# Optimization experiments

Measured on AMD Instinct MI355X. Metric: run time of the kernel, lower is better.

## Reference

```python
import jax, jax.numpy as jnp
import numpy as np

B, NB, K, S = 4, 131072, 32, 768


def setup_inputs() -> dict:
    key = jax.random.key(0)
    k1, k2, k3, k4 = jax.random.split(key, 4)
    N = B * NB
    logits_embedding = jax.random.normal(k1, (N, 4), dtype=jnp.float32)
    logits_seediness = jax.random.normal(k2, (N, 1), dtype=jnp.float32)
    coords = jax.random.uniform(k3, (N, 3), dtype=jnp.float32, minval=0.0, maxval=float(S))
    inst = jax.random.randint(k4, (N,), 0, K).astype(jnp.float32)
    batch = jnp.repeat(jnp.arange(B, dtype=jnp.float32), NB)
    labels = jnp.concatenate(
        [batch[:, None], coords, jnp.zeros((N, 1), jnp.float32), inst[:, None]], axis=1)
    return {"logits_embedding": logits_embedding,
            "logits_seediness": logits_seediness,
            "labels": labels}


def reference(logits_embedding, logits_seediness, labels):
    half = S / 2.0
    # coords_embedding = emb[:, :3] + (voxel_coords - S/2) / (S/2)
    ce = logits_embedding[:, :3] + (labels[:, 1:4] - half) / half          # [N,3]
    sigma = logits_embedding[:, 3]                                          # [N]
    seed = logits_seediness.reshape(-1)                                     # [N]
    inst = labels[:, 5].astype(jnp.int32)                                   # [N]

    # batch ids are contiguous by construction -> reshape to [B, NB, ...]
    ce = ce.reshape(B, NB, 3)
    sigma = sigma.reshape(B, NB)
    seed = seed.reshape(B, NB)
    inst = inst.reshape(B, NB)

    onehot = (inst[:, :, None] == jnp.arange(K)[None, None, :]).astype(jnp.float32)  # [B,NB,K]
    counts = jnp.maximum(onehot.sum(axis=1), 1.0)                                    # [B,K]

    centers = jnp.einsum('bnk,bnd->bkd', onehot, ce) / counts[:, :, None]            # [B,K,3]
    sigmas = jnp.einsum('bnk,bn->bk', onehot, sigma) / counts                        # [B,K]

    # squared distance of every point to every instance center
    diff = ce[:, :, None, :] - centers[:, None, :, :]                                # [B,NB,K,3]
    dist2 = jnp.sum(diff * diff, axis=-1)                                            # [B,NB,K]

    arg = jnp.clip(dist2 / (2.0 * sigmas[:, None, :] ** 2), 1e-7, 100.0)
    p = jnp.exp(-arg)                                                                # [B,NB,K]

    # mask loss: log(p) == -arg exactly
    mask_loss = -(onehot * (-arg) + (1.0 - onehot) * jnp.log1p(-p)).sum(axis=(1, 2)) / NB / K  # [B]

    smooth = (onehot * jnp.abs(sigma[:, :, None] - sigmas[:, None, :])).sum(axis=1) / counts
    smooth_loss = smooth.sum(axis=1) / K                                             # [B]

    seed_term = (onehot * (seed[:, :, None] - p) ** 2).sum(axis=1) / counts
    seed_loss = seed_term.sum(axis=1) / K                                            # [B]

    # inter-cluster hinge, sum over unordered pairs i<j, denom K*(K-1)
    cdiff = centers[:, :, None, :] - centers[:, None, :, :]                          # [B,K,K,3]
    cd2 = jnp.sum(cdiff * cdiff, axis=-1)
    eye = jnp.eye(K, dtype=jnp.float32)[None]
    d = jnp.sqrt(jnp.where(eye > 0, 1.0, cd2))                                       # safe sqrt on diag
    hinge = jnp.maximum(0.0, 2.0 * 0.5 - d) ** 2 * (1.0 - eye)
    inter_loss = hinge.sum(axis=(1, 2)) / 2.0 / (K * (K - 1))                        # [B]

    loss = jnp.mean(mask_loss + smooth_loss + inter_loss + seed_loss)

    # accuracy: assign each point to nearest center (instance ids are 0..K-1)
    pred = jnp.argmin(dist2, axis=2)                                                 # [B,NB]
    acc = jnp.mean((pred == inst).astype(jnp.float32))
    return loss, jax.lax.stop_gradient(acc)
```

## Files before the change

### kernel.cpp

```cpp
#include <hip/hip_runtime.h>

#define B_ 4
#define NB_ 131072
#define K_ 32
#define N_ (B_*NB_)
#define BK_ (B_*K_)
#define NACC 256
#define ABLK 64
#define PTS_PER_ACC 2048

#define ACC_OFF  0
#define FIN_OFF  (NACC*5*K_)
#define PART_OFF (FIN_OFF + 6*BK_)

__global__ __launch_bounds__(1024) void k_accum(
    const float4* __restrict__ emb, const float* __restrict__ labels,
    float* __restrict__ ws)
{
    __shared__ float sacc[5*K_];
    int tid = threadIdx.x;
    if (tid < 5*K_) sacc[tid] = 0.f;
    __syncthreads();
    int start = blockIdx.x * PTS_PER_ACC;
    #pragma unroll
    for (int i = 0; i < PTS_PER_ACC/1024; ++i) {
        int n = start + i*1024 + tid;
        float4 e = emb[n];
        const float* lr = labels + (size_t)n*6;
        float c1 = lr[1];
        float2 c23 = *reinterpret_cast<const float2*>(lr + 2);
        int inst = ((int)lr[5]) & 31;
        float cex = e.x + (c1    - 384.f)/384.f;
        float cey = e.y + (c23.x - 384.f)/384.f;
        float cez = e.z + (c23.y - 384.f)/384.f;
        atomicAdd(&sacc[0*K_+inst], cex);
        atomicAdd(&sacc[1*K_+inst], cey);
        atomicAdd(&sacc[2*K_+inst], cez);
        atomicAdd(&sacc[3*K_+inst], e.w);
        atomicAdd(&sacc[4*K_+inst], 1.0f);
    }
    __syncthreads();
    if (tid < 5*K_) ws[ACC_OFF + blockIdx.x*5*K_ + tid] = sacc[tid];
}

__global__ __launch_bounds__(256) void k_main(
    const float4* __restrict__ emb, const float* __restrict__ seedp,
    const float* __restrict__ labels, float* __restrict__ ws,
    float4* __restrict__ part)
{
    __shared__ float s_raw[5*K_];
    __shared__ float s_cx[K_], s_cy[K_], s_cz[K_], s_sig[K_], s_inv[K_], s_i2s[K_];
    int tid = threadIdx.x;
    int n = blockIdx.x * 256 + tid;
    int b = blockIdx.x >> 9;

    if (tid < 5*K_) {
        float a = 0.f;
        const float* base = ws + ACC_OFF + (size_t)b*ABLK*5*K_ + tid;
        #pragma unroll 8
        for (int j = 0; j < ABLK; ++j) a += base[(size_t)j*5*K_];
        s_raw[tid] = a;
    }
    __syncthreads();
    if (tid < K_) {
        float cnt = fmaxf(s_raw[4*K_+tid], 1.f);
        float inv = 1.f / cnt;
        float cx = s_raw[0*K_+tid] * inv;
        float cy = s_raw[1*K_+tid] * inv;
        float cz = s_raw[2*K_+tid] * inv;
        float sg = s_raw[3*K_+tid] * inv;
        float i2s = 1.f / (2.f*sg*sg);
        s_cx[tid] = cx;  s_cy[tid] = cy;  s_cz[tid] = cz;
        s_sig[tid] = sg; s_inv[tid] = inv; s_i2s[tid] = i2s;
        if ((blockIdx.x & 511) == 0) {
            float* fin = ws + FIN_OFF;
            fin[0*BK_ + b*K_+tid] = cx;
            fin[1*BK_ + b*K_+tid] = cy;
            fin[2*BK_ + b*K_+tid] = cz;
            fin[3*BK_ + b*K_+tid] = sg;
            fin[4*BK_ + b*K_+tid] = inv;
            fin[5*BK_ + b*K_+tid] = i2s;
        }
    }
    __syncthreads();

    float4 e = emb[n];
    float sd = seedp[n];
    const float* lr = labels + (size_t)n*6;
    float c1 = lr[1];
    float2 c23 = *reinterpret_cast<const float2*>(lr + 2);
    int inst = ((int)lr[5]) & 31;
    float cex = e.x + (c1    - 384.f)/384.f;
    float cey = e.y + (c23.x - 384.f)/384.f;
    float cez = e.z + (c23.y - 384.f)/384.f;
    float sigma = e.w;

    unsigned bestpk = 0xffffffffu;
    float minarg = 3.4e38f;
    #pragma unroll
    for (int k = 0; k < K_; ++k) {
        float dx = cex - s_cx[k];
        float dy = cey - s_cy[k];
        float dz = cez - s_cz[k];
        float d2 = dx*dx + dy*dy + dz*dz;
        unsigned pk = (__float_as_uint(d2) & ~31u) | (unsigned)k;
        bestpk = min(bestpk, pk);
        minarg = fminf(minarg, d2 * s_i2s[k]);
    }
    int bi = (int)(bestpk & 31u);

    float msum = 0.f;
    if (__any(minarg < 17.f)) {
        #pragma unroll 4
        for (int k = 0; k < K_; ++k) {
            float dx = cex - s_cx[k];
            float dy = cey - s_cy[k];
            float dz = cez - s_cz[k];
            float d2 = dx*dx + dy*dy + dz*dz;
            float arg = d2 * s_i2s[k];
            if (arg < 17.f) {
                float argc = fmaxf(arg, 1e-7f);
                float p = __expf(-argc);
                msum += __logf(1.f - p);
            }
        }
    }

    float dxI = cex - s_cx[inst];
    float dyI = cey - s_cy[inst];
    float dzI = cez - s_cz[inst];
    float d2I = dxI*dxI + dyI*dyI + dzI*dzI;
    float argRawI = d2I * s_i2s[inst];
    float argI = fminf(fmaxf(argRawI, 1e-7f), 100.f);
    float pI = __expf(-argI);
    if (argRawI < 17.f) msum -= __logf(1.f - pI);
    msum -= argI;

    float inv_in = s_inv[inst];
    float smoothv = fabsf(sigma - s_sig[inst]) * inv_in;
    float dsd = sd - pI;
    float seedv = dsd*dsd*inv_in;
    float accv = (bi == inst) ? 1.0f : 0.0f;

    float v0 = msum, v1 = smoothv, v2 = seedv, v3 = accv;
    for (int off = 32; off; off >>= 1) {
        v0 += __shfl_down(v0, off);
        v1 += __shfl_down(v1, off);
        v2 += __shfl_down(v2, off);
        v3 += __shfl_down(v3, off);
    }
    __shared__ float sred[4][4];
    int wid = tid >> 6, lane = tid & 63;
    if (lane == 0) { sred[wid][0]=v0; sred[wid][1]=v1; sred[wid][2]=v2; sred[wid][3]=v3; }
    __syncthreads();
    if (tid == 0) {
        float r0=0.f,r1=0.f,r2=0.f,r3=0.f;
        for (int w = 0; w < 4; ++w) { r0+=sred[w][0]; r1+=sred[w][1]; r2+=sred[w][2]; r3+=sred[w][3]; }
        part[blockIdx.x] = make_float4(r0, r1, r2, r3);
    }
}

__global__ __launch_bounds__(256) void k_final(
    const float* __restrict__ ws, const float* __restrict__ part,
    float* __restrict__ out)
{
    int tid = threadIdx.x;

    int pair = tid >> 4;
    int lane16 = tid & 15;
    int f = pair >> 2, b = pair & 3;
    float v = 0.f;
    #pragma unroll
    for (int j = 0; j < 32; ++j) {
        int blk = b*512 + lane16*32 + j;
        v += part[blk*4 + f];
    }
    v += __shfl_down(v, 8);
    v += __shfl_down(v, 4);
    v += __shfl_down(v, 2);
    v += __shfl_down(v, 1);
    __shared__ float S[16];
    if (lane16 == 0) S[pair] = v;

    float h = 0.f;
    for (int idx = tid; idx < B_*K_*K_; idx += 256) {
        int bb = idx >> 10;
        int ij = idx & 1023;
        int i = ij >> 5, j = ij & 31;
        if (i != j) {
            const float* fin = ws + FIN_OFF;
            float dx = fin[0*BK_ + bb*K_+i] - fin[0*BK_ + bb*K_+j];
            float dy = fin[1*BK_ + bb*K_+i] - fin[1*BK_ + bb*K_+j];
            float dz = fin[2*BK_ + bb*K_+i] - fin[2*BK_ + bb*K_+j];
            float cd2 = dx*dx + dy*dy + dz*dz;
            float d = sqrtf(cd2);
            float hg = fmaxf(0.f, 1.0f - d);
            h += hg*hg;
        }
    }
    for (int off = 32; off; off >>= 1) h += __shfl_down(h, off);
    __shared__ float sh[4];
    int wid = tid >> 6, lane = tid & 63;
    if (lane == 0) sh[wid] = h;
    __syncthreads();

    if (tid == 0) {
        float ht = sh[0]+sh[1]+sh[2]+sh[3];
        float loss = 0.f;
        for (int bb = 0; bb < B_; ++bb) {
            float mask_l   = -S[0*4+bb] / (float)NB_ / (float)K_;
            float smooth_l =  S[1*4+bb] / (float)K_;
            float seed_l   =  S[2*4+bb] / (float)K_;
            loss += mask_l + smooth_l + seed_l;
        }
        loss = loss / (float)B_ + ht / (2.0f * (float)(K_*(K_-1)) * (float)B_);
        float acc = (S[3*4+0]+S[3*4+1]+S[3*4+2]+S[3*4+3]) / (float)N_;
        out[0] = loss;
        out[1] = acc;
    }
}

extern "C" void kernel_launch(void* const* d_in, const int* in_sizes, int n_in,
                              void* d_out, int out_size, void* d_ws, size_t ws_size,
                              hipStream_t stream)
{
    const float4* emb    = (const float4*)d_in[0];
    const float*  seedp  = (const float*)d_in[1];
    const float*  labels = (const float*)d_in[2];
    float* ws  = (float*)d_ws;
    float* out = (float*)d_out;

    k_accum <<<NACC,   1024, 0, stream>>>(emb, labels, ws);
    k_main  <<<N_/256, 256,  0, stream>>>(emb, seedp, labels, ws,
                                          (float4*)(ws + PART_OFF));
    k_final <<<1,      256,  0, stream>>>(ws, ws + PART_OFF, out);
}
```

Baseline: 46.23 us.

## Cache packed embeddings and instance ids in workspace; add per-batch center finalize kernel

k_accum now writes a packed float4 (center-offset embedding plus sigma) and a byte instance id per point to workspace. k_main reads these instead of re-reading the embedding and the strided 24-byte label rows. A new 4-block k_finalize kernel computes the centers once per batch, so every k_main block no longer re-reduces 64 partial accumulators. The trade is an extra ~10 MB of writes in k_accum and one more kernel launch, in exchange for lighter reads and a shorter prologue in k_main.

```diff
diff --git a/kernel.cpp b/kernel.cpp
--- a/kernel.cpp
+++ b/kernel.cpp
@@ -12,11 +12,15 @@
 #define ACC_OFF  0
 #define FIN_OFF  (NACC*5*K_)
 #define PART_OFF (FIN_OFF + 6*BK_)
+#define PK_OFF   49920
+#define INST_OFF (PK_OFF + N_*4)
 
 __global__ __launch_bounds__(1024) void k_accum(
     const float4* __restrict__ emb, const float* __restrict__ labels,
     float* __restrict__ ws)
 {
+    float4* pk = (float4*)(ws + PK_OFF);
+    unsigned char* inst8 = (unsigned char*)(ws + INST_OFF);
     __shared__ float sacc[5*K_];
     int tid = threadIdx.x;
     if (tid < 5*K_) sacc[tid] = 0.f;
@@ -33,6 +37,8 @@
         float cex = e.x + (c1    - 384.f)/384.f;
         float cey = e.y + (c23.x - 384.f)/384.f;
         float cez = e.z + (c23.y - 384.f)/384.f;
+        pk[n] = make_float4(cex, cey, cez, e.w);
+        inst8[n] = (unsigned char)inst;
         atomicAdd(&sacc[0*K_+inst], cex);
         atomicAdd(&sacc[1*K_+inst], cey);
         atomicAdd(&sacc[2*K_+inst], cez);
@@ -43,17 +49,11 @@
     if (tid < 5*K_) ws[ACC_OFF + blockIdx.x*5*K_ + tid] = sacc[tid];
 }
 
-__global__ __launch_bounds__(256) void k_main(
-    const float4* __restrict__ emb, const float* __restrict__ seedp,
-    const float* __restrict__ labels, float* __restrict__ ws,
-    float4* __restrict__ part)
-{
+__global__ __launch_bounds__(256) void k_finalize(float* __restrict__ ws)
+{
+    int b = blockIdx.x;
+    int tid = threadIdx.x;
     __shared__ float s_raw[5*K_];
-    __shared__ float s_cx[K_], s_cy[K_], s_cz[K_], s_sig[K_], s_inv[K_], s_i2s[K_];
-    int tid = threadIdx.x;
-    int n = blockIdx.x * 256 + tid;
-    int b = blockIdx.x >> 9;
-
     if (tid < 5*K_) {
         float a = 0.f;
         const float* base = ws + ACC_OFF + (size_t)b*ABLK*5*K_ + tid;
@@ -70,30 +70,44 @@
         float cz = s_raw[2*K_+tid] * inv;
         float sg = s_raw[3*K_+tid] * inv;
         float i2s = 1.f / (2.f*sg*sg);
-        s_cx[tid] = cx;  s_cy[tid] = cy;  s_cz[tid] = cz;
-        s_sig[tid] = sg; s_inv[tid] = inv; s_i2s[tid] = i2s;
-        if ((blockIdx.x & 511) == 0) {
-            float* fin = ws + FIN_OFF;
-            fin[0*BK_ + b*K_+tid] = cx;
-            fin[1*BK_ + b*K_+tid] = cy;
-            fin[2*BK_ + b*K_+tid] = cz;
-            fin[3*BK_ + b*K_+tid] = sg;
-            fin[4*BK_ + b*K_+tid] = inv;
-            fin[5*BK_ + b*K_+tid] = i2s;
-        }
-    }
-    __syncthreads();
-
-    float4 e = emb[n];
+        float* fin = ws + FIN_OFF;
+        fin[0*BK_ + b*K_+tid] = cx;
+        fin[1*BK_ + b*K_+tid] = cy;
+        fin[2*BK_ + b*K_+tid] = cz;
+        fin[3*BK_ + b*K_+tid] = sg;
+        fin[4*BK_ + b*K_+tid] = inv;
+        fin[5*BK_ + b*K_+tid] = i2s;
+    }
+}
+
+__global__ __launch_bounds__(256) void k_main(
+    const float4* __restrict__ emb, const float* __restrict__ seedp,
+    const float* __restrict__ labels, float* __restrict__ ws,
+    float4* __restrict__ part)
+{
+    __shared__ float s_all[6*K_];
+    int tid = threadIdx.x;
+    int n = blockIdx.x * 256 + tid;
+    int b = blockIdx.x >> 9;
+    const float4* pk = (const float4*)(ws + PK_OFF);
+    const unsigned char* inst8 = (const unsigned char*)(ws + INST_OFF);
+
+    if (tid < 6*K_) {
+        int f = tid >> 5, k = tid & 31;
+        s_all[tid] = ws[FIN_OFF + f*BK_ + b*K_ + k];
+    }
+    __syncthreads();
+    const float* s_cx  = s_all + 0*K_;
+    const float* s_cy  = s_all + 1*K_;
+    const float* s_cz  = s_all + 2*K_;
+    const float* s_sig = s_all + 3*K_;
+    const float* s_inv = s_all + 4*K_;
+    const float* s_i2s = s_all + 5*K_;
+
+    float4 p4 = pk[n];
     float sd = seedp[n];
-    const float* lr = labels + (size_t)n*6;
-    float c1 = lr[1];
-    float2 c23 = *reinterpret_cast<const float2*>(lr + 2);
-    int inst = ((int)lr[5]) & 31;
-    float cex = e.x + (c1    - 384.f)/384.f;
-    float cey = e.y + (c23.x - 384.f)/384.f;
-    float cez = e.z + (c23.y - 384.f)/384.f;
-    float sigma = e.w;
+    int inst = (int)inst8[n];
+    float cex = p4.x, cey = p4.y, cez = p4.z, sigma = p4.w;
 
     unsigned bestpk = 0xffffffffu;
     float minarg = 3.4e38f;
@@ -103,8 +117,8 @@
         float dy = cey - s_cy[k];
         float dz = cez - s_cz[k];
         float d2 = dx*dx + dy*dy + dz*dz;
-        unsigned pk = (__float_as_uint(d2) & ~31u) | (unsigned)k;
-        bestpk = min(bestpk, pk);
+        unsigned pkb = (__float_as_uint(d2) & ~31u) | (unsigned)k;
+        bestpk = min(bestpk, pkb);
         minarg = fminf(minarg, d2 * s_i2s[k]);
     }
     int bi = (int)(bestpk & 31u);
@@ -230,8 +244,9 @@
     float* ws  = (float*)d_ws;
     float* out = (float*)d_out;
 
-    k_accum <<<NACC,   1024, 0, stream>>>(emb, labels, ws);
-    k_main  <<<N_/256, 256,  0, stream>>>(emb, seedp, labels, ws,
-                                          (float4*)(ws + PART_OFF));
-    k_final <<<1,      256,  0, stream>>>(ws, ws + PART_OFF, out);
-}
+    k_accum    <<<NACC,   1024, 0, stream>>>(emb, labels, ws);
+    k_finalize <<<B_,     256,  0, stream>>>(ws);
+    k_main     <<<N_/256, 256,  0, stream>>>(emb, seedp, labels, ws,
+                                             (float4*)(ws + PART_OFF));
+    k_final    <<<1,      256,  0, stream>>>(ws, ws + PART_OFF, out);
+}
```

New measurement: 44.75 us. 3.2% less time.
